# Kernel optimization log

Hardware: AMD Instinct MI355X
Metric: run time of the kernel (lower is better)

## Reference

```python
import jax, jax.numpy as jnp
import numpy as np

VOCAB = 50000
D = 256        # embedding_dim = nb_head * size_per_head
H = 8          # nb_head
DH = 32        # size_per_head
B = 8192
L = 64


def setup_inputs() -> dict:
    key = jax.random.key(0)
    ks = jax.random.split(key, 8)
    tokens = jax.random.randint(ks[0], (B, L), 0, VOCAB)
    scale = 0.02
    emb_table = jax.random.normal(ks[1], (VOCAB, D), dtype=jnp.float32) * scale
    WQ = jax.random.normal(ks[2], (D, D), dtype=jnp.float32) * scale
    WK = jax.random.normal(ks[3], (D, D), dtype=jnp.float32) * scale
    WV = jax.random.normal(ks[4], (D, D), dtype=jnp.float32) * scale
    WO = jax.random.normal(ks[5], (D, D), dtype=jnp.float32) * scale
    dense_w = jax.random.normal(ks[6], (D, 1), dtype=jnp.float32) * scale
    dense_b = jnp.zeros((1,), dtype=jnp.float32)
    return {"tokens": tokens, "emb_table": emb_table, "WQ": WQ, "WK": WK,
            "WV": WV, "WO": WO, "dense_w": dense_w, "dense_b": dense_b}


def _fastformer(x, WQ, WK, WV, WO):
    # x: [B, L, D]
    b, l, _ = x.shape
    Q = (x @ WQ).reshape(b, l, H, DH)
    K = (x @ WK).reshape(b, l, H, DH)
    V = (x @ WV).reshape(b, l, H, DH)
    global_q = jnp.mean(Q, axis=1, keepdims=True)   # [B,1,H,DH]
    global_k = jnp.mean(K, axis=1, keepdims=True)
    w = jnp.sum(global_q * K + global_k * Q, axis=-1)  # [B,L,H]
    w = jax.nn.softmax(w, axis=1)                       # softmax over seq
    context = (w[..., None] * V).reshape(b, l, D)
    return context @ WO


def reference(tokens, emb_table, WQ, WK, WV, WO, dense_w, dense_b):
    # NewsEncoder forward (inference: dropout = identity; masks computed but
    # unused by Fastformer.call, matching the original code).
    title_emb = emb_table[tokens]                       # [B,L,D]
    hidden = _fastformer(title_emb, WQ, WK, WV, WO)     # [B,L,D]
    scores = (hidden @ dense_w + dense_b)[..., 0]       # [B,L]
    attn = jax.nn.softmax(scores, axis=1)               # over seq
    news_vector = jnp.sum(hidden * attn[..., None], axis=1)  # [B,D]
    return news_vector
```

## Files before the change

kernel.cpp:

```cpp
#include <hip/hip_runtime.h>
#include <cstdint>


using f32x4  = __attribute__((ext_vector_type(4))) float;
using bf16x8 = __attribute__((ext_vector_type(8))) short;

__device__ __forceinline__ unsigned int pack2bf(float a, float b) {
  unsigned int ua = __builtin_bit_cast(unsigned int, a);
  unsigned int ub = __builtin_bit_cast(unsigned int, b);
  ua = (ua + 0x7fffu + ((ua >> 16) & 1u)) >> 16;
  ub = (ub + 0x7fffu + ((ub >> 16) & 1u)) >> 16;
  return ua | (ub << 16);
}
__device__ __forceinline__ unsigned short bf1(float a) {
  unsigned int ua = __builtin_bit_cast(unsigned int, a);
  ua = (ua + 0x7fffu + ((ua >> 16) & 1u)) >> 16;
  return (unsigned short)ua;
}
__device__ __forceinline__ float ubf(unsigned int u) {
  return __builtin_bit_cast(float, u << 16);
}

__global__ __launch_bounds__(256) void prep_kernel(const float* __restrict__ WV,
                                                   const float* __restrict__ WO,
                                                   const float* __restrict__ dw,
                                                   unsigned short* __restrict__ mbf) {
  __shared__ float wod[256];
  const int t = threadIdx.x;
  float acc = 0.f;
  for (int e = 0; e < 256; e += 4) {
    const float4 w4 = *(const float4*)(WO + (size_t)t * 256 + e);
    const float4 d4 = *(const float4*)(dw + e);
    acc += w4.x * d4.x + w4.y * d4.y + w4.z * d4.z + w4.w * d4.w;
  }
  wod[t] = acc;
  __syncthreads();
  for (int h = 0; h < 8; ++h) {
    float a = 0.f;
    for (int j = 0; j < 32; j += 4) {
      const float4 w4 = *(const float4*)(WV + (size_t)t * 256 + h * 32 + j);
      a += w4.x * wod[h*32+j] + w4.y * wod[h*32+j+1] + w4.z * wod[h*32+j+2] + w4.w * wod[h*32+j+3];
    }
    const float o = __shfl_xor(a, 1);
    if (!(t & 1)) ((unsigned int*)mbf)[h * 128 + (t >> 1)] = pack2bf(a, o);
  }
}

__global__ __launch_bounds__(256) void prep_T(const float* __restrict__ WQ,
                                              const float* __restrict__ WK,
                                              unsigned short* __restrict__ tkn) {
  __shared__ float ek[8][32], eq[8][32];
  const int t = threadIdx.x;
  const int n0 = blockIdx.x * 8;
  const int h  = n0 >> 8;
  {
    const int ei = t >> 5, j = t & 31;
    const int e = (n0 & 255) + ei;
    ek[ei][j] = WK[(size_t)e * 256 + h * 32 + j];
    eq[ei][j] = WQ[(size_t)e * 256 + h * 32 + j];
  }
  __syncthreads();
  float wqd[32], wkd[32];
#pragma unroll
  for (int j = 0; j < 32; j += 4) {
    *(float4*)(wqd + j) = *(const float4*)(WQ + (size_t)t * 256 + h * 32 + j);
    *(float4*)(wkd + j) = *(const float4*)(WK + (size_t)t * 256 + h * 32 + j);
  }
#pragma unroll
  for (int ei = 0; ei < 8; ++ei) {
    float a = 0.f;
#pragma unroll
    for (int j = 0; j < 32; ++j) a += wqd[j] * ek[ei][j] + wkd[j] * eq[ei][j];
    const float o = __shfl_xor(a, 1);
    if (!(t & 1)) ((unsigned int*)tkn)[(size_t)(n0 + ei) * 128 + (t >> 1)] = pack2bf(a, o);
  }
}

__global__ __launch_bounds__(256) void ebf_kernel(const float4* __restrict__ emb4,
                                                  uint2* __restrict__ out2, int n) {
  for (int i = blockIdx.x * 256 + threadIdx.x; i < n; i += gridDim.x * 256) {
    const float4 v = emb4[i];
    uint2 pk;
    pk.x = pack2bf(v.x, v.y);
    pk.y = pack2bf(v.z, v.w);
    out2[i] = pk;
  }
}

__global__ __launch_bounds__(256) void xbar_kernel(const int* __restrict__ tokens,
                                                   const unsigned short* __restrict__ ebf,
                                                   unsigned short* __restrict__ xbf) {
  __shared__ int tok[64];
  __shared__ float part[4][64][4];
  const int b = blockIdx.x, t = threadIdx.x;
  if (t < 64) tok[t] = tokens[b * 64 + t];
  __syncthreads();
  const int cp = t & 63, rg = t >> 6;
  const uint2* e2 = (const uint2*)ebf;
  float s0 = 0.f, s1 = 0.f, s2 = 0.f, s3 = 0.f;
#pragma unroll
  for (int ri = 0; ri < 16; ++ri) {
    const uint2 u = e2[(size_t)tok[rg * 16 + ri] * 64 + cp];
    s0 += ubf(u.x & 0xffffu); s1 += ubf(u.x >> 16);
    s2 += ubf(u.y & 0xffffu); s3 += ubf(u.y >> 16);
  }
  *(float4*)part[rg][cp] = make_float4(s0, s1, s2, s3);
  __syncthreads();
  if (t < 64) {
    const float4 p0 = *(const float4*)part[0][t];
    const float4 p1 = *(const float4*)part[1][t];
    const float4 p2 = *(const float4*)part[2][t];
    const float4 p3 = *(const float4*)part[3][t];
    const float a0 = (p0.x + p1.x + p2.x + p3.x) * (1.f / 64.f);
    const float a1 = (p0.y + p1.y + p2.y + p3.y) * (1.f / 64.f);
    const float a2 = (p0.z + p1.z + p2.z + p3.z) * (1.f / 64.f);
    const float a3 = (p0.w + p1.w + p2.w + p3.w) * (1.f / 64.f);
    uint2 pk;
    pk.x = pack2bf(a0, a1);
    pk.y = pack2bf(a2, a3);
    *(uint2*)((unsigned int*)xbf + (size_t)b * 128 + 2 * t) = pk;
  }
}

__global__ __launch_bounds__(256) void cgemm(const unsigned short* __restrict__ xbf,
                                             const unsigned short* __restrict__ tkn,
                                             unsigned short* __restrict__ cbf) {
  __shared__ unsigned short As[64 * 264];
  const int t = threadIdx.x;
  const int m0 = blockIdx.x * 64, n0 = blockIdx.y * 64;
#pragma unroll
  for (int it = 0; it < 8; ++it) {
    const int idx = it * 256 + t;
    const int row = idx >> 5, c = idx & 31;
    const uint4 v = *(const uint4*)(xbf + (size_t)(m0 + row) * 256 + c * 8);
    *(uint4*)(As + row * 264 + c * 8) = v;
  }
  __syncthreads();
  const int wv = t >> 6, l = t & 63;
  const int g = l >> 4, r = l & 15;
#pragma unroll
  for (int nt = 0; nt < 4; ++nt) {
    const int n = n0 + nt * 16 + r;
    f32x4 acc = {0.f, 0.f, 0.f, 0.f};
#pragma unroll
    for (int kk = 0; kk < 8; ++kk) {
      const bf16x8 a  = *(const bf16x8*)(As + (16 * wv + r) * 264 + kk * 32 + g * 8);
      const bf16x8 bb = *(const bf16x8*)(tkn + (size_t)n * 256 + kk * 32 + g * 8);
      acc = __builtin_amdgcn_mfma_f32_16x16x32_bf16(a, bb, acc, 0, 0, 0);
    }
#pragma unroll
    for (int i = 0; i < 4; ++i)
      cbf[(size_t)(m0 + 16 * wv + g * 4 + i) * 2048 + n] = bf1(acc[i]);
  }
}

__global__ __launch_bounds__(256) void main_kernel(const int* __restrict__ tokens,
                                                   const unsigned short* __restrict__ ebf,
                                                   const unsigned short* __restrict__ mbf,
                                                   const float* __restrict__ dense_b,
                                                   unsigned short* __restrict__ cbf) {
  __shared__ unsigned short xl[64 * 264];
  __shared__ float wslds[64 * 17];
  const int t = threadIdx.x;
  const int b = blockIdx.x;
  const int wv = t >> 6, l = t & 63;
  const int g = l >> 4, r = l & 15;
  {
    const uint4* eb4 = (const uint4*)ebf;
#pragma unroll
    for (int it = 0; it < 8; ++it) {
      const int idx = it * 256 + t;
      const int row = idx >> 5, c = idx & 31;
      const int tk = tokens[b * 64 + row];
      *(uint4*)(xl + row * 264 + c * 8) = eb4[(size_t)tk * 32 + c];
    }
  }
  __syncthreads();
  {
    const unsigned short* arow = xl + (16 * wv + r) * 264;
    const unsigned short* brow = (r < 8) ? (cbf + (size_t)b * 2048 + r * 256)
                                         : (mbf + (size_t)(r - 8) * 256);
    f32x4 acc = {0.f, 0.f, 0.f, 0.f};
#pragma unroll
    for (int kk = 0; kk < 8; ++kk) {
      const bf16x8 a  = *(const bf16x8*)(arow + kk * 32 + g * 8);
      const bf16x8 bb = *(const bf16x8*)(brow + kk * 32 + g * 8);
      acc = __builtin_amdgcn_mfma_f32_16x16x32_bf16(a, bb, acc, 0, 0, 0);
    }
#pragma unroll
    for (int i = 0; i < 4; ++i)
      wslds[(16 * wv + g * 4 + i) * 17 + r] = acc[i];
  }
  __syncthreads();
  {
#pragma unroll
    for (int hh = 0; hh < 2; ++hh) {
      const int h = 2 * wv + hh;
      const float v = wslds[l * 17 + h];
      float mx = v;
#pragma unroll
      for (int sft = 32; sft; sft >>= 1) mx = fmaxf(mx, __shfl_xor(mx, sft));
      const float e = expf(v - mx);
      float sm = e;
#pragma unroll
      for (int sft = 32; sft; sft >>= 1) sm += __shfl_xor(sm, sft);
      wslds[l * 17 + h] = e / sm;
    }
  }
  __syncthreads();
  float cc0, cc1;
  {
    float p[8], sv[8];
#pragma unroll
    for (int h = 0; h < 8; ++h) { p[h] = wslds[l*17 + h]; sv[h] = wslds[l*17 + 8 + h]; }
    float sc = dense_b[0];
#pragma unroll
    for (int h = 0; h < 8; ++h) sc += p[h] * sv[h];
    float mx = sc;
#pragma unroll
    for (int sft = 32; sft; sft >>= 1) mx = fmaxf(mx, __shfl_xor(mx, sft));
    const float e = expf(sc - mx);
    float sm = e;
#pragma unroll
    for (int sft = 32; sft; sft >>= 1) sm += __shfl_xor(sm, sft);
    const float attn = e / sm;
    float co[8];
#pragma unroll
    for (int h = 0; h < 8; ++h) co[h] = attn * p[h];
    if      (wv == 0) { cc0 = co[0]; cc1 = co[1]; }
    else if (wv == 1) { cc0 = co[2]; cc1 = co[3]; }
    else if (wv == 2) { cc0 = co[4]; cc1 = co[5]; }
    else              { cc0 = co[6]; cc1 = co[7]; }
  }
  {
    const unsigned int* xu = (const unsigned int*)xl;
    float y0[4] = {}, y1[4] = {};
#pragma unroll
    for (int ll = 0; ll < 64; ++ll) {
      const uint2 xv = *(const uint2*)(xu + ll * 132 + l * 2);
      const float c0 = __shfl(cc0, ll);
      const float c1 = __shfl(cc1, ll);
      const float x0 = ubf(xv.x & 0xffffu);
      const float x1 = ubf(xv.x >> 16);
      const float x2 = ubf(xv.y & 0xffffu);
      const float x3 = ubf(xv.y >> 16);
      y0[0] += c0 * x0; y0[1] += c0 * x1; y0[2] += c0 * x2; y0[3] += c0 * x3;
      y1[0] += c1 * x0; y1[1] += c1 * x1; y1[2] += c1 * x2; y1[3] += c1 * x3;
    }
    uint2 pk0, pk1;
    pk0.x = pack2bf(y0[0], y0[1]); pk0.y = pack2bf(y0[2], y0[3]);
    pk1.x = pack2bf(y1[0], y1[1]); pk1.y = pack2bf(y1[2], y1[3]);
    *(uint2*)(cbf + (size_t)b * 2048 + (2 * wv) * 256 + l * 4)     = pk0;
    *(uint2*)(cbf + (size_t)b * 2048 + (2 * wv + 1) * 256 + l * 4) = pk1;
  }
}

template <bool A_BF16>
__global__ __launch_bounds__(256) void gemm_t(const void* __restrict__ Av,
                                              const float* __restrict__ Bm,
                                              float* __restrict__ C,
                                              int N, int K, int lda, int ldb, int ldc,
                                              long aZ, long bZ, long cZ) {
  __shared__ float As[64 * 20];
  __shared__ float Bs[16 * 68];
  const int t = threadIdx.x;
  const int bm = blockIdx.x * 64, bn = blockIdx.y * 64;
  Bm += (long)blockIdx.z * bZ;
  C  += (long)blockIdx.z * cZ;
  const int ty = t >> 4, tx = t & 15;
  const int lr = t >> 2, lj = (t & 3) * 4;
  const int lk = t >> 4, ln = (t & 15) * 4;
  float acc[4][4] = {};
  for (int k0 = 0; k0 < K; k0 += 16) {
    float4 a4;
    if constexpr (A_BF16) {
      const unsigned short* A = (const unsigned short*)Av + (long)blockIdx.z * aZ;
      const uint2 au = *(const uint2*)(A + (size_t)(bm + lr) * lda + k0 + lj);
      a4 = make_float4(ubf(au.x & 0xffffu), ubf(au.x >> 16),
                       ubf(au.y & 0xffffu), ubf(au.y >> 16));
    } else {
      const float* A = (const float*)Av + (long)blockIdx.z * aZ;
      a4 = *(const float4*)(A + (size_t)(bm + lr) * lda + k0 + lj);
    }
    float4 b4 = make_float4(0.f, 0.f, 0.f, 0.f);
    if (bn + ln < N) b4 = *(const float4*)(Bm + (size_t)(k0 + lk) * ldb + bn + ln);
    __syncthreads();
    *(float4*)(As + lr * 20 + lj) = a4;
    *(float4*)(Bs + lk * 68 + ln) = b4;
    __syncthreads();
#pragma unroll
    for (int k = 0; k < 16; ++k) {
      const float a0 = As[(4*ty+0)*20 + k];
      const float a1 = As[(4*ty+1)*20 + k];
      const float a2 = As[(4*ty+2)*20 + k];
      const float a3 = As[(4*ty+3)*20 + k];
      const float4 bb = *(const float4*)(Bs + k * 68 + 4 * tx);
      acc[0][0]+=a0*bb.x; acc[0][1]+=a0*bb.y; acc[0][2]+=a0*bb.z; acc[0][3]+=a0*bb.w;
      acc[1][0]+=a1*bb.x; acc[1][1]+=a1*bb.y; acc[1][2]+=a1*bb.z; acc[1][3]+=a1*bb.w;
      acc[2][0]+=a2*bb.x; acc[2][1]+=a2*bb.y; acc[2][2]+=a2*bb.z; acc[2][3]+=a2*bb.w;
      acc[3][0]+=a3*bb.x; acc[3][1]+=a3*bb.y; acc[3][2]+=a3*bb.z; acc[3][3]+=a3*bb.w;
    }
  }
  if (bn + 4 * tx < N) {
#pragma unroll
    for (int i = 0; i < 4; ++i) {
      *(float4*)(C + (size_t)(bm + 4*ty + i) * ldc + bn + 4*tx) =
          make_float4(acc[i][0], acc[i][1], acc[i][2], acc[i][3]);
    }
  }
}

extern "C" void kernel_launch(void* const* d_in, const int* in_sizes, int n_in,
                              void* d_out, int out_size, void* d_ws, size_t ws_size,
                              hipStream_t stream) {
  const int*   tokens = (const int*)d_in[0];
  const float* emb    = (const float*)d_in[1];
  const float* WQ     = (const float*)d_in[2];
  const float* WK     = (const float*)d_in[3];
  const float* WV     = (const float*)d_in[4];
  const float* WO     = (const float*)d_in[5];
  const float* dw     = (const float*)d_in[6];
  const float* db     = (const float*)d_in[7];
  float* out = (float*)d_out;

  unsigned short* base = (unsigned short*)d_ws;
  unsigned short* mbf  = base;
  unsigned short* xbf  = base + 2048;
  unsigned short* tkn  = xbf + (size_t)8192 * 256;
  unsigned short* cbf  = tkn + (size_t)2048 * 256;
  unsigned short* ebf  = cbf + (size_t)8192 * 2048;
  float* cbar = (float*)ebf;

  const size_t need_bytes = (size_t)(2048 + 8192*256 + 2048*256 + 8192*2048
                                     + 50000*256) * 2;
  if (ws_size < need_bytes) return;

  prep_kernel<<<dim3(1), dim3(256), 0, stream>>>(WV, WO, dw, mbf);
  prep_T<<<dim3(256), dim3(256), 0, stream>>>(WQ, WK, tkn);
  ebf_kernel<<<dim3(2048), dim3(256), 0, stream>>>((const float4*)emb, (uint2*)ebf,
                                                   50000 * 64);
  xbar_kernel<<<dim3(8192), dim3(256), 0, stream>>>(tokens, ebf, xbf);
  cgemm<<<dim3(128, 32), dim3(256), 0, stream>>>(xbf, tkn, cbf);
  main_kernel<<<dim3(8192), dim3(256), 0, stream>>>(tokens, ebf, mbf, db, cbf);
  gemm_t<true><<<dim3(128, 1, 8), dim3(256), 0, stream>>>(cbf, WV, cbar, 32, 256, 2048, 256, 256, 256l, 32l, 32l);
  gemm_t<false><<<dim3(128, 4, 1), dim3(256), 0, stream>>>(cbar, WO, out, 256, 256, 256, 256, 256, 0l, 0l, 0l);
}
```

Before: 283.6 us.

## Fold WV and WO into one per-head projection and apply it with bf16 MFMA

```diff
diff --git a/kernel.cpp b/kernel.cpp
--- a/kernel.cpp
+++ b/kernel.cpp
@@ -73,6 +73,34 @@
     for (int j = 0; j < 32; ++j) a += wqd[j] * ek[ei][j] + wkd[j] * eq[ei][j];
     const float o = __shfl_xor(a, 1);
     if (!(t & 1)) ((unsigned int*)tkn)[(size_t)(n0 + ei) * 128 + (t >> 1)] = pack2bf(a, o);
+  }
+}
+
+__global__ __launch_bounds__(256) void prep_P(const float* __restrict__ WV,
+                                              const float* __restrict__ WO,
+                                              unsigned short* __restrict__ ptb) {
+  __shared__ float wvs[32][32];
+  __shared__ float wos[32][256];
+  const int t = threadIdx.x;
+  const int h = blockIdx.x, d0 = blockIdx.y * 32;
+  {
+    const int dd = t >> 3, jq = (t & 7) * 4;
+    *(float4*)(&wvs[dd][jq]) = *(const float4*)(WV + (size_t)(d0 + dd) * 256 + h * 32 + jq);
+    const int c4 = (t & 63) * 4;
+#pragma unroll
+    for (int jj = 0; jj < 8; ++jj) {
+      const int j = (t >> 6) * 8 + jj;
+      *(float4*)(&wos[j][c4]) = *(const float4*)(WO + (size_t)(h * 32 + j) * 256 + c4);
+    }
+  }
+  __syncthreads();
+  const int n = t;
+#pragma unroll 4
+  for (int dd = 0; dd < 32; ++dd) {
+    float a = 0.f;
+#pragma unroll
+    for (int j = 0; j < 32; ++j) a += wvs[dd][j] * wos[j][n];
+    ptb[(size_t)n * 2048 + h * 256 + d0 + dd] = bf1(a);
   }
 }
 
@@ -255,58 +283,44 @@
   }
 }
 
-template <bool A_BF16>
-__global__ __launch_bounds__(256) void gemm_t(const void* __restrict__ Av,
-                                              const float* __restrict__ Bm,
-                                              float* __restrict__ C,
-                                              int N, int K, int lda, int ldb, int ldc,
-                                              long aZ, long bZ, long cZ) {
-  __shared__ float As[64 * 20];
-  __shared__ float Bs[16 * 68];
-  const int t = threadIdx.x;
-  const int bm = blockIdx.x * 64, bn = blockIdx.y * 64;
-  Bm += (long)blockIdx.z * bZ;
-  C  += (long)blockIdx.z * cZ;
-  const int ty = t >> 4, tx = t & 15;
-  const int lr = t >> 2, lj = (t & 3) * 4;
-  const int lk = t >> 4, ln = (t & 15) * 4;
-  float acc[4][4] = {};
-  for (int k0 = 0; k0 < K; k0 += 16) {
-    float4 a4;
-    if constexpr (A_BF16) {
-      const unsigned short* A = (const unsigned short*)Av + (long)blockIdx.z * aZ;
-      const uint2 au = *(const uint2*)(A + (size_t)(bm + lr) * lda + k0 + lj);
-      a4 = make_float4(ubf(au.x & 0xffffu), ubf(au.x >> 16),
-                       ubf(au.y & 0xffffu), ubf(au.y >> 16));
-    } else {
-      const float* A = (const float*)Av + (long)blockIdx.z * aZ;
-      a4 = *(const float4*)(A + (size_t)(bm + lr) * lda + k0 + lj);
-    }
-    float4 b4 = make_float4(0.f, 0.f, 0.f, 0.f);
-    if (bn + ln < N) b4 = *(const float4*)(Bm + (size_t)(k0 + lk) * ldb + bn + ln);
+__global__ __launch_bounds__(256) void pgemm(const unsigned short* __restrict__ cbf,
+                                             const unsigned short* __restrict__ ptb,
+                                             float* __restrict__ out) {
+  __shared__ unsigned short As[32 * 264];
+  const int t = threadIdx.x;
+  const int m0 = blockIdx.x * 32;
+  const int wv = t >> 6, l = t & 63;
+  const int g = l >> 4, r = l & 15;
+  const int mt = wv & 1;
+  const int ng0 = (wv >> 1) * 8;
+  f32x4 acc[8] = {};
+  for (int kc = 0; kc < 8; ++kc) {
+#pragma unroll
+    for (int it = 0; it < 4; ++it) {
+      const int idx = it * 256 + t;
+      const int row = idx >> 5, c = idx & 31;
+      const uint4 v = *(const uint4*)(cbf + (size_t)(m0 + row) * 2048 + kc * 256 + c * 8);
+      *(uint4*)(As + row * 264 + c * 8) = v;
+    }
     __syncthreads();
-    *(float4*)(As + lr * 20 + lj) = a4;
-    *(float4*)(Bs + lk * 68 + ln) = b4;
+#pragma unroll
+    for (int kk = 0; kk < 8; ++kk) {
+      const bf16x8 a = *(const bf16x8*)(As + (16 * mt + r) * 264 + kk * 32 + g * 8);
+#pragma unroll
+      for (int nt = 0; nt < 8; ++nt) {
+        const int n = (ng0 + nt) * 16 + r;
+        const bf16x8 bb = *(const bf16x8*)(ptb + (size_t)n * 2048 + kc * 256 + kk * 32 + g * 8);
+        acc[nt] = __builtin_amdgcn_mfma_f32_16x16x32_bf16(a, bb, acc[nt], 0, 0, 0);
+      }
+    }
     __syncthreads();
-#pragma unroll
-    for (int k = 0; k < 16; ++k) {
-      const float a0 = As[(4*ty+0)*20 + k];
-      const float a1 = As[(4*ty+1)*20 + k];
-      const float a2 = As[(4*ty+2)*20 + k];
-      const float a3 = As[(4*ty+3)*20 + k];
-      const float4 bb = *(const float4*)(Bs + k * 68 + 4 * tx);
-      acc[0][0]+=a0*bb.x; acc[0][1]+=a0*bb.y; acc[0][2]+=a0*bb.z; acc[0][3]+=a0*bb.w;
-      acc[1][0]+=a1*bb.x; acc[1][1]+=a1*bb.y; acc[1][2]+=a1*bb.z; acc[1][3]+=a1*bb.w;
-      acc[2][0]+=a2*bb.x; acc[2][1]+=a2*bb.y; acc[2][2]+=a2*bb.z; acc[2][3]+=a2*bb.w;
-      acc[3][0]+=a3*bb.x; acc[3][1]+=a3*bb.y; acc[3][2]+=a3*bb.z; acc[3][3]+=a3*bb.w;
-    }
-  }
-  if (bn + 4 * tx < N) {
-#pragma unroll
-    for (int i = 0; i < 4; ++i) {
-      *(float4*)(C + (size_t)(bm + 4*ty + i) * ldc + bn + 4*tx) =
-          make_float4(acc[i][0], acc[i][1], acc[i][2], acc[i][3]);
-    }
+  }
+#pragma unroll
+  for (int nt = 0; nt < 8; ++nt) {
+    const int n = (ng0 + nt) * 16 + r;
+#pragma unroll
+    for (int i = 0; i < 4; ++i)
+      out[(size_t)(m0 + 16 * mt + g * 4 + i) * 256 + n] = acc[nt][i];
   }
 }
 
@@ -329,19 +343,19 @@
   unsigned short* tkn  = xbf + (size_t)8192 * 256;
   unsigned short* cbf  = tkn + (size_t)2048 * 256;
   unsigned short* ebf  = cbf + (size_t)8192 * 2048;
-  float* cbar = (float*)ebf;
+  unsigned short* ptb  = ebf + (size_t)50000 * 256;
 
   const size_t need_bytes = (size_t)(2048 + 8192*256 + 2048*256 + 8192*2048
-                                     + 50000*256) * 2;
+                                     + 50000*256 + 256*2048) * 2;
   if (ws_size < need_bytes) return;
 
   prep_kernel<<<dim3(1), dim3(256), 0, stream>>>(WV, WO, dw, mbf);
   prep_T<<<dim3(256), dim3(256), 0, stream>>>(WQ, WK, tkn);
+  prep_P<<<dim3(8, 8), dim3(256), 0, stream>>>(WV, WO, ptb);
   ebf_kernel<<<dim3(2048), dim3(256), 0, stream>>>((const float4*)emb, (uint2*)ebf,
                                                    50000 * 64);
   xbar_kernel<<<dim3(8192), dim3(256), 0, stream>>>(tokens, ebf, xbf);
   cgemm<<<dim3(128, 32), dim3(256), 0, stream>>>(xbf, tkn, cbf);
   main_kernel<<<dim3(8192), dim3(256), 0, stream>>>(tokens, ebf, mbf, db, cbf);
-  gemm_t<true><<<dim3(128, 1, 8), dim3(256), 0, stream>>>(cbf, WV, cbar, 32, 256, 2048, 256, 256, 256l, 32l, 32l);
-  gemm_t<false><<<dim3(128, 4, 1), dim3(256), 0, stream>>>(cbar, WO, out, 256, 256, 256, 256, 256, 0l, 0l, 0l);
-}
+  pgemm<<<dim3(256), dim3(256), 0, stream>>>(cbf, ptb, out);
+}
```

Result: slower. 357.6 us (+26.1%).
